# Optimization experiments

Hardware: AMD Instinct MI355X
Metric: run time of the kernel (lower is better)

The kernel has to match this reference:

```python
import jax, jax.numpy as jnp
import numpy as np
import math

B, N, F0, HID, OUT, K = 8, 2048, 128, 64, 16, 10


def setup_inputs() -> dict:
    key = jax.random.key(0)
    ks = jax.random.split(key, 6)
    X = jax.random.normal(ks[0], (B, N, F0), dtype=jnp.float32)
    # Row-stochastic dense 'rescaled Laplacian': spectrum inside unit disk,
    # so K-th order Bernstein polynomial stays numerically stable.
    A = jax.random.uniform(ks[1], (N, N), dtype=jnp.float32)
    L = A / jnp.sum(A, axis=1, keepdims=True)
    W1 = jax.random.normal(ks[2], (F0, HID), dtype=jnp.float32) / np.float32(np.sqrt(F0))
    b1 = jnp.zeros((HID,), dtype=jnp.float32)
    W2 = jax.random.normal(ks[3], (HID, OUT), dtype=jnp.float32) / np.float32(np.sqrt(HID))
    b2 = jnp.zeros((OUT,), dtype=jnp.float32)
    theta = 0.02 * jax.random.normal(ks[4], (K + 1,), dtype=jnp.float32)
    return {"X": X, "L": L, "W1": W1, "b1": b1, "W2": W2, "b2": b2,
            "theta": theta, "dp": 0}


def _bern_filter(Hf, L, theta, binom):
    # g(L) Hf = sum_i theta_i C(K,i) L^i (I-L)^{K-i} Hf
    # Computed by applying L / (I-L) directly to the (B,N,F) features
    # (mathematically identical to forming the NxN basis matrices).
    Lap = lambda Y: jnp.einsum('vw,bwf->bvf', L, Y)
    ys = [Hf]                       # ys[k] = (I-L)^k Hf
    for _ in range(K):
        ys.append(ys[-1] - Lap(ys[-1]))
    a = theta * binom               # (K+1,)
    # Horner in L: r = a_K Hf; r <- L r + a_i (I-L)^{K-i} Hf
    r = a[K] * Hf
    for i in range(K - 1, -1, -1):
        r = Lap(r) + a[i] * ys[K - i]
    return r


def reference(X, L, W1, b1, W2, b2, theta, dp):
    binom = jnp.asarray([math.comb(K, i) for i in range(K + 1)], dtype=X.dtype)
    # dropout with p=dp=0 is identity
    Hf = jax.nn.relu(X @ W1 + b1)          # (B, N, HID)
    Hf = _bern_filter(Hf, L, theta, binom) # (B, N, HID)
    Hg = jnp.mean(Hf, axis=1)              # (B, HID)
    logits = Hg @ W2 + b2                  # (B, OUT)
    return logits
```

## Files before the change

### kernel.cpp

```cpp
#include <hip/hip_runtime.h>

#define NN     2048
#define F0D    128
#define HIDD   64
#define OUTD   16
#define KDEG   10
#define NCHAIN 128
#define COLS   16

typedef unsigned int u32;

#define CTAG(j) (0xC0DE0000u + (u32)(j))
#define HTAG    0xBEEF0001u

static __device__ __forceinline__ u32 ld_flag(const u32* p) {
    return __hip_atomic_load(p, __ATOMIC_RELAXED, __HIP_MEMORY_SCOPE_AGENT);
}
static __device__ __forceinline__ void st_flag(u32* p, u32 v) {
    __hip_atomic_store(p, v, __ATOMIC_RELAXED, __HIP_MEMORY_SCOPE_AGENT);
}
static __device__ __forceinline__ void st_data(float* p, float v) {
    __hip_atomic_store(p, v, __ATOMIC_RELAXED, __HIP_MEMORY_SCOPE_AGENT);
}

__global__ __launch_bounds__(256, 1) void k_fused(
    const float* __restrict__ X, const float* __restrict__ L,
    const float* __restrict__ W1, const float* __restrict__ b1,
    const float* __restrict__ W2, const float* __restrict__ b2,
    const float* __restrict__ theta, float* __restrict__ out,
    float* __restrict__ ws)
{
    float* PB  = ws;
    float* HP  = ws + 20480;
    u32*   FLC = (u32*)(ws + 28672);
    u32*   FLH = (u32*)(ws + 49152);

    __shared__ union {
        struct { float Lt[NN * COLS]; float xs[NN]; float redf[4][16]; float cbv[16]; } mv;
        struct { float W1t[64][132]; float redm[16][65]; float wv[64]; } hd;
    } sm;

    const int g = blockIdx.x;
    const int t = threadIdx.x;

    if (g < NCHAIN) {
        const int u0 = g * COLS;

        if (t <= KDEG) {
            const float C10[11] = {1,10,45,120,210,252,210,120,45,10,1};
            float acc = 0.f;
            for (int i = 0; i <= t; ++i) {
                int n = KDEG - i, r = t - i;
                long long cm = 1;
                for (int s = 1; s <= r; ++s) cm = cm * (n - r + s) / s;
                float term = theta[i] * C10[i] * (float)cm;
                if ((t - i) & 1) term = -term;
                acc += term;
            }
            sm.mv.cbv[t] = acc;
        }

        const float4* L4  = (const float4*)L;
        float4*       Lt4 = (float4*)sm.mv.Lt;
        const int qc = t & 3, r0 = t >> 2;
        float4 acc = make_float4(0.f, 0.f, 0.f, 0.f);
        #pragma unroll 8
        for (int i = 0; i < 32; ++i) {
            int v = r0 + 64 * i;
            float4 lv = L4[(size_t)v * (NN / 4) + (u0 >> 2) + qc];
            Lt4[v * 4 + qc] = lv;
            acc.x += lv.x; acc.y += lv.y; acc.z += lv.z; acc.w += lv.w;
        }
        #pragma unroll
        for (int m = 4; m <= 32; m <<= 1) {
            acc.x += __shfl_xor(acc.x, m); acc.y += __shfl_xor(acc.y, m);
            acc.z += __shfl_xor(acc.z, m); acc.w += __shfl_xor(acc.w, m);
        }
        {
            int lane = t & 63, wid = t >> 6;
            if (lane < 4) *(float4*)&sm.mv.redf[wid][lane * 4] = acc;
        }
        __syncthreads();

        float wacc = 0.f;
        if (t < COLS) {
            float s = sm.mv.redf[0][t] + sm.mv.redf[1][t]
                    + sm.mv.redf[2][t] + sm.mv.redf[3][t];
            wacc = sm.mv.cbv[0];
            st_data(&PB[u0 + t], s);
        }
        if (t < 64) {
            asm volatile("s_waitcnt vmcnt(0)" ::: "memory");
            if (t == 0) st_flag(((u32*)(ws + 28672)) + g * 16, CTAG(1));
        }

        for (int j = 2; j <= KDEG; ++j) {
            if (t < 32) {
                const u32* fb = (u32*)(ws + 28672 + (size_t)(j - 2) * 2048);
                const u32 tag = CTAG(j - 1);
                u32 need = 0xFu;
                while (need) {
                    #pragma unroll
                    for (int i = 0; i < 4; ++i)
                        if (need & (1u << i))
                            if (ld_flag(fb + (t + 32 * i) * 16) == tag)
                                need &= ~(1u << i);
                    if (need) __builtin_amdgcn_s_sleep(1);
                }
            }
            __syncthreads();

            const float4* src4 = (const float4*)(PB + (size_t)(j - 2) * 2048);
            float4* xs4 = (float4*)sm.mv.xs;
            xs4[t]       = src4[t];
            xs4[t + 256] = src4[t + 256];
            __syncthreads();

            float pprev = (t < COLS) ? sm.mv.xs[u0 + t] : 0.f;

            float4 a2 = make_float4(0.f, 0.f, 0.f, 0.f);
            #pragma unroll 8
            for (int k = 0; k < 32; ++k) {
                int v = r0 + 64 * k;
                float xv = sm.mv.xs[v];
                float4 lv = Lt4[v * 4 + qc];
                a2.x += lv.x * xv; a2.y += lv.y * xv;
                a2.z += lv.z * xv; a2.w += lv.w * xv;
            }
            #pragma unroll
            for (int m = 4; m <= 32; m <<= 1) {
                a2.x += __shfl_xor(a2.x, m); a2.y += __shfl_xor(a2.y, m);
                a2.z += __shfl_xor(a2.z, m); a2.w += __shfl_xor(a2.w, m);
            }
            {
                int lane = t & 63, wid = t >> 6;
                if (lane < 4) *(float4*)&sm.mv.redf[wid][lane * 4] = a2;
            }
            __syncthreads();

            if (t < COLS) {
                float s = sm.mv.redf[0][t] + sm.mv.redf[1][t]
                        + sm.mv.redf[2][t] + sm.mv.redf[3][t];
                wacc += sm.mv.cbv[j - 1] * pprev;
                float val = (j < KDEG) ? s : (wacc + sm.mv.cbv[KDEG] * s);
                st_data(&PB[(size_t)(j - 1) * 2048 + u0 + t], val);
            }
            if (t < 64) {
                asm volatile("s_waitcnt vmcnt(0)" ::: "memory");
                if (t == 0)
                    st_flag(((u32*)(ws + 28672 + (size_t)(j - 1) * 2048)) + g * 16,
                            CTAG(j));
            }
        }

        if (g == 0) {
            if (t < 32) {
                u32 need = 0xFu;
                while (need) {
                    #pragma unroll
                    for (int i = 0; i < 4; ++i)
                        if (need & (1u << i))
                            if (ld_flag(FLH + (t + 32 * i) * 16) == HTAG)
                                need &= ~(1u << i);
                    if (need) __builtin_amdgcn_s_sleep(2);
                }
            }
            __syncthreads();
            float s2[2];
            #pragma unroll
            for (int e = 0; e < 2; ++e) {
                int idx = t * 2 + e, b = idx >> 6, h = idx & 63;
                const float* hp = HP + (size_t)(b * 32) * 64 + h;
                float ss = 0.f;
                #pragma unroll
                for (int vc = 0; vc < 32; ++vc) ss += hp[vc * 64];
                s2[e] = ss;
            }
            sm.mv.xs[t * 2]     = s2[0];
            sm.mv.xs[t * 2 + 1] = s2[1];
            __syncthreads();
            if (t < 128) {
                int o = t & 15, bb = t >> 4;
                float a3 = b2[o];
                #pragma unroll
                for (int h = 0; h < HIDD; ++h)
                    a3 += sm.mv.xs[bb * 64 + h] * W2[h * 16 + o];
                out[bb * 16 + o] = a3;
            }
        }
        return;
    }

    const int u = g - NCHAIN;
    const int vchunk = u & 31, bA = u >> 5, bB = bA + 4;

    for (int i = t; i < F0D * HIDD; i += 256) {
        int f = i >> 6, h = i & 63;
        sm.hd.W1t[h][f] = W1[i];
    }
    __syncthreads();

    const int hg = t & 15, vg = t >> 4;
    const int vbase = vchunk * 64 + vg * 4;
    const float* XA = X + ((size_t)bA * NN + vbase) * F0D;
    const float* XB = X + ((size_t)bB * NN + vbase) * F0D;
    float accA[4][4] = {}, accB[4][4] = {};
    for (int f = 0; f < F0D; f += 4) {
        float4 xa[4], xb[4];
        #pragma unroll
        for (int i = 0; i < 4; ++i) {
            xa[i] = *(const float4*)(XA + (size_t)i * F0D + f);
            xb[i] = *(const float4*)(XB + (size_t)i * F0D + f);
        }
        #pragma unroll
        for (int jj = 0; jj < 4; ++jj) {
            float4 wr = *(const float4*)(&sm.hd.W1t[hg + 16 * jj][f]);
            #pragma unroll
            for (int i = 0; i < 4; ++i) {
                accA[i][jj] += xa[i].x * wr.x + xa[i].y * wr.y
                             + xa[i].z * wr.z + xa[i].w * wr.w;
                accB[i][jj] += xb[i].x * wr.x + xb[i].y * wr.y
                             + xb[i].z * wr.z + xb[i].w * wr.w;
            }
        }
    }

    if (t < 4) {
        const u32* fp = ((u32*)(ws + 28672 + (size_t)(KDEG - 1) * 2048))
                      + (vchunk * 4 + t) * 16;
        while (ld_flag(fp) != CTAG(KDEG)) __builtin_amdgcn_s_sleep(2);
    }
    __syncthreads();
    if (t < 16)
        ((float4*)sm.hd.wv)[t] =
            ((const float4*)(PB + (size_t)(KDEG - 1) * 2048 + vchunk * 64))[t];
    __syncthreads();

    const float inv = 1.0f / (float)NN;
    float hsA[4] = {0.f,0.f,0.f,0.f}, hsB[4] = {0.f,0.f,0.f,0.f};
    #pragma unroll
    for (int i = 0; i < 4; ++i) {
        float we = sm.hd.wv[vg * 4 + i];
        #pragma unroll
        for (int jj = 0; jj < 4; ++jj) {
            float rA = accA[i][jj] + b1[hg + 16 * jj];
            float rB = accB[i][jj] + b1[hg + 16 * jj];
            rA = rA > 0.f ? rA : 0.f;
            rB = rB > 0.f ? rB : 0.f;
            hsA[jj] += rA * we;
            hsB[jj] += rB * we;
        }
    }
    #pragma unroll
    for (int jj = 0; jj < 4; ++jj) sm.hd.redm[vg][hg + 16 * jj] = hsA[jj];
    __syncthreads();
    if (t < 64) {
        float s = 0.f;
        #pragma unroll
        for (int i = 0; i < 16; ++i) s += sm.hd.redm[i][t];
        st_data(&HP[(size_t)(bA * 32 + vchunk) * 64 + t], s * inv);
    }
    __syncthreads();
    #pragma unroll
    for (int jj = 0; jj < 4; ++jj) sm.hd.redm[vg][hg + 16 * jj] = hsB[jj];
    __syncthreads();
    if (t < 64) {
        float s = 0.f;
        #pragma unroll
        for (int i = 0; i < 16; ++i) s += sm.hd.redm[i][t];
        st_data(&HP[(size_t)(bB * 32 + vchunk) * 64 + t], s * inv);
    }
    if (t < 64) {
        asm volatile("s_waitcnt vmcnt(0)" ::: "memory");
        if (t == 0) st_flag(FLH + u * 16, HTAG);
    }
}

extern "C" void kernel_launch(void* const* d_in, const int* in_sizes, int n_in,
                              void* d_out, int out_size, void* d_ws, size_t ws_size,
                              hipStream_t stream) {
    const float* X     = (const float*)d_in[0];
    const float* L     = (const float*)d_in[1];
    const float* W1    = (const float*)d_in[2];
    const float* b1    = (const float*)d_in[3];
    const float* W2    = (const float*)d_in[4];
    const float* b2    = (const float*)d_in[5];
    const float* theta = (const float*)d_in[6];
    float* outp = (float*)d_out;
    float* wsp  = (float*)d_ws;

    hipLaunchKernelGGL(k_fused, dim3(256), dim3(256), 0, stream,
                       X, L, W1, b1, W2, b2, theta, outp, wsp);
}
```

Measured before the change: 123.4 us.

## Replace block barriers and LDS staging with wave-vote flag polling in chain loop

Each chain step used to poll the flags with 32 threads, hit a block barrier, copy the previous 2048-entry vector into LDS, and hit a second barrier. Now one wave polls all 128 flags with a wave-wide vote and raises an LDS ready word that the other waves spin on, and each thread reads the previous vector straight from global memory. The previous column value is carried in a register instead of being re-read. Separately, the feature (HP) blocks now wait until the chain blocks have published their first step before starting, and HP is moved to a new workspace offset. The aim is to cut per-step barrier and copy latency on the serial K-step chain, at the cost of uncached global reads inside the inner loop and spin-waiting.

```diff
diff --git a/kernel.cpp b/kernel.cpp
--- a/kernel.cpp
+++ b/kernel.cpp
@@ -31,12 +31,11 @@
     float* __restrict__ ws)
 {
     float* PB  = ws;
-    float* HP  = ws + 20480;
-    u32*   FLC = (u32*)(ws + 28672);
     u32*   FLH = (u32*)(ws + 49152);
+    float* HP  = ws + 51200;
 
     __shared__ union {
-        struct { float Lt[NN * COLS]; float xs[NN]; float redf[4][16]; float cbv[16]; } mv;
+        struct { float Lt[NN * COLS]; float redf[4][16]; float cbv[16]; int rdy[16]; } mv;
         struct { float W1t[64][132]; float redm[16][65]; float wv[64]; } hd;
     } sm;
 
@@ -59,34 +58,35 @@
             }
             sm.mv.cbv[t] = acc;
         }
+        if (t < 16) sm.mv.rdy[t] = 0;
 
         const float4* L4  = (const float4*)L;
         float4*       Lt4 = (float4*)sm.mv.Lt;
         const int qc = t & 3, r0 = t >> 2;
-        float4 acc = make_float4(0.f, 0.f, 0.f, 0.f);
-        #pragma unroll 8
-        for (int i = 0; i < 32; ++i) {
-            int v = r0 + 64 * i;
-            float4 lv = L4[(size_t)v * (NN / 4) + (u0 >> 2) + qc];
-            Lt4[v * 4 + qc] = lv;
-            acc.x += lv.x; acc.y += lv.y; acc.z += lv.z; acc.w += lv.w;
-        }
-        #pragma unroll
-        for (int m = 4; m <= 32; m <<= 1) {
-            acc.x += __shfl_xor(acc.x, m); acc.y += __shfl_xor(acc.y, m);
-            acc.z += __shfl_xor(acc.z, m); acc.w += __shfl_xor(acc.w, m);
-        }
         {
+            float4 acc = make_float4(0.f, 0.f, 0.f, 0.f);
+            #pragma unroll 8
+            for (int i = 0; i < 32; ++i) {
+                int v = r0 + 64 * i;
+                float4 lv = L4[(size_t)v * (NN / 4) + (u0 >> 2) + qc];
+                Lt4[v * 4 + qc] = lv;
+                acc.x += lv.x; acc.y += lv.y; acc.z += lv.z; acc.w += lv.w;
+            }
+            #pragma unroll
+            for (int m = 4; m <= 32; m <<= 1) {
+                acc.x += __shfl_xor(acc.x, m); acc.y += __shfl_xor(acc.y, m);
+                acc.z += __shfl_xor(acc.z, m); acc.w += __shfl_xor(acc.w, m);
+            }
             int lane = t & 63, wid = t >> 6;
             if (lane < 4) *(float4*)&sm.mv.redf[wid][lane * 4] = acc;
         }
         __syncthreads();
 
-        float wacc = 0.f;
+        float val = 0.f, wacc = 0.f;
         if (t < COLS) {
             float s = sm.mv.redf[0][t] + sm.mv.redf[1][t]
                     + sm.mv.redf[2][t] + sm.mv.redf[3][t];
-            wacc = sm.mv.cbv[0];
+            val = s; wacc = sm.mv.cbv[0];
             st_data(&PB[u0 + t], s);
         }
         if (t < 64) {
@@ -95,34 +95,27 @@
         }
 
         for (int j = 2; j <= KDEG; ++j) {
-            if (t < 32) {
-                const u32* fb = (u32*)(ws + 28672 + (size_t)(j - 2) * 2048);
+            if (t < 64) {
+                const u32* fb = (const u32*)(ws + 28672 + (size_t)(j - 2) * 2048);
                 const u32 tag = CTAG(j - 1);
-                u32 need = 0xFu;
-                while (need) {
-                    #pragma unroll
-                    for (int i = 0; i < 4; ++i)
-                        if (need & (1u << i))
-                            if (ld_flag(fb + (t + 32 * i) * 16) == tag)
-                                need &= ~(1u << i);
-                    if (need) __builtin_amdgcn_s_sleep(1);
-                }
-            }
-            __syncthreads();
-
-            const float4* src4 = (const float4*)(PB + (size_t)(j - 2) * 2048);
-            float4* xs4 = (float4*)sm.mv.xs;
-            xs4[t]       = src4[t];
-            xs4[t + 256] = src4[t + 256];
-            __syncthreads();
-
-            float pprev = (t < COLS) ? sm.mv.xs[u0 + t] : 0.f;
-
+                const u32* f0 = fb + t * 16;
+                const u32* f1 = fb + (t + 64) * 16;
+                while (!__all(ld_flag(f0) == tag && ld_flag(f1) == tag))
+                    __builtin_amdgcn_s_sleep(1);
+                asm volatile("" ::: "memory");
+                if (t == 0) ((volatile int*)sm.mv.rdy)[j] = 1;
+            } else {
+                volatile int* vr = (volatile int*)sm.mv.rdy;
+                while (vr[j] == 0) __builtin_amdgcn_s_sleep(1);
+                asm volatile("" ::: "memory");
+            }
+
+            const float* psrc = PB + (size_t)(j - 2) * 2048;
             float4 a2 = make_float4(0.f, 0.f, 0.f, 0.f);
             #pragma unroll 8
             for (int k = 0; k < 32; ++k) {
                 int v = r0 + 64 * k;
-                float xv = sm.mv.xs[v];
+                float xv = psrc[v];
                 float4 lv = Lt4[v * 4 + qc];
                 a2.x += lv.x * xv; a2.y += lv.y * xv;
                 a2.z += lv.z * xv; a2.w += lv.w * xv;
@@ -141,9 +134,10 @@
             if (t < COLS) {
                 float s = sm.mv.redf[0][t] + sm.mv.redf[1][t]
                         + sm.mv.redf[2][t] + sm.mv.redf[3][t];
-                wacc += sm.mv.cbv[j - 1] * pprev;
-                float val = (j < KDEG) ? s : (wacc + sm.mv.cbv[KDEG] * s);
-                st_data(&PB[(size_t)(j - 1) * 2048 + u0 + t], val);
+                wacc += sm.mv.cbv[j - 1] * val;
+                val = s;
+                float outv = (j < KDEG) ? s : (wacc + sm.mv.cbv[KDEG] * s);
+                st_data(&PB[(size_t)(j - 1) * 2048 + u0 + t], outv);
             }
             if (t < 64) {
                 asm volatile("s_waitcnt vmcnt(0)" ::: "memory");
@@ -164,6 +158,7 @@
                                 need &= ~(1u << i);
                     if (need) __builtin_amdgcn_s_sleep(2);
                 }
+                asm volatile("" ::: "memory");
             }
             __syncthreads();
             float s2[2];
@@ -176,15 +171,15 @@
                 for (int vc = 0; vc < 32; ++vc) ss += hp[vc * 64];
                 s2[e] = ss;
             }
-            sm.mv.xs[t * 2]     = s2[0];
-            sm.mv.xs[t * 2 + 1] = s2[1];
+            sm.mv.Lt[t * 2]     = s2[0];
+            sm.mv.Lt[t * 2 + 1] = s2[1];
             __syncthreads();
             if (t < 128) {
                 int o = t & 15, bb = t >> 4;
                 float a3 = b2[o];
                 #pragma unroll
                 for (int h = 0; h < HIDD; ++h)
-                    a3 += sm.mv.xs[bb * 64 + h] * W2[h * 16 + o];
+                    a3 += sm.mv.Lt[bb * 64 + h] * W2[h * 16 + o];
                 out[bb * 16 + o] = a3;
             }
         }
@@ -193,6 +188,12 @@
 
     const int u = g - NCHAIN;
     const int vchunk = u & 31, bA = u >> 5, bB = bA + 4;
+
+    if (t == 0) {
+        const u32* fp = ((const u32*)(ws + 28672)) + u * 16;
+        while (ld_flag(fp) != CTAG(1)) __builtin_amdgcn_s_sleep(2);
+    }
+    __syncthreads();
 
     for (int i = t; i < F0D * HIDD; i += 256) {
         int f = i >> 6, h = i & 63;
@@ -229,6 +230,7 @@
         const u32* fp = ((u32*)(ws + 28672 + (size_t)(KDEG - 1) * 2048))
                       + (vchunk * 4 + t) * 16;
         while (ld_flag(fp) != CTAG(KDEG)) __builtin_amdgcn_s_sleep(2);
+        asm volatile("" ::: "memory");
     }
     __syncthreads();
     if (t < 16)
```

Result: no change. 123.4 us (+0.1%).
